# Performance work log

Hardware: AMD Instinct MI355X
Metric: run time of the kernel (lower is better)

## Reference

```python
import jax, jax.numpy as jnp
import numpy as np

SCALE = 0.125  # 1/sqrt(d_head=64)

def setup_inputs() -> dict:
    key = jax.random.key(0)
    kq, kk, kv = jax.random.split(key, 3)
    shape = (2, 12, 2048, 64)  # [batch, heads, seq, d_head]
    q = jax.random.normal(kq, shape, dtype=jnp.float32)
    k = jax.random.normal(kk, shape, dtype=jnp.float32)
    v = jax.random.normal(kv, shape, dtype=jnp.float32)
    return {"q": q, "k": k, "v": v}

def reference(q, k, v) -> jnp.ndarray:
    # atten = softmax(q @ k^T * scale); res = atten @ v
    scores = jnp.einsum('bhik,bhjk->bhij', q, k) * SCALE  # [B,H,S,S]
    atten = jax.nn.softmax(scores, axis=-1)
    # dropout is Identity (atten_dropout=None)
    res = jnp.einsum('bhij,bhjd->bhid', atten, v)  # [B,H,S,D]
    return res
```

## Files before the change

kernel.cpp:

```cpp
#include <hip/hip_runtime.h>
#include <math.h>

#define SEQ   2048
#define DH    64
#define NBH   24
#define QSCALE 0.18033688011112042f

typedef __attribute__((ext_vector_type(8))) short short8;
typedef __attribute__((ext_vector_type(4))) short short4v;
typedef __attribute__((ext_vector_type(4))) float f32x4;

#define MFMA32(a, b, c) __builtin_amdgcn_mfma_f32_16x16x32_bf16((a), (b), (c), 0, 0, 0)
#define MFMA16(a, b, c) __builtin_amdgcn_mfma_f32_16x16x16bf16_1k((a), (b), (c), 0, 0, 0)

__device__ __forceinline__ int cvtpk(float lo, float hi) {
    int r;
    asm("v_cvt_pk_bf16_f32 %0, %1, %2" : "=v"(r) : "v"(lo), "v"(hi));
    return r;
}

__global__ __launch_bounds__(256)
void cvt_all(const float* __restrict__ q, const float* __restrict__ k,
             const float* __restrict__ v,
             short* __restrict__ qb, short* __restrict__ kb,
             short* __restrict__ vt)
{
    __shared__ float tile[32][68];
    const int t  = threadIdx.x;
    const int bh = blockIdx.x;
    const int s0 = blockIdx.y * 32;
    const size_t base = ((size_t)bh * SEQ + s0) * DH;
    const size_t kbh  = (size_t)bh * SEQ * DH;

    #pragma unroll
    for (int i = 0; i < 2; ++i) {
        const int idx = i * 256 + t;
        float4 a = ((const float4*)(q + base))[idx];
        ((int2*)(qb + base))[idx] = make_int2(
            cvtpk(a.x * QSCALE, a.y * QSCALE),
            cvtpk(a.z * QSCALE, a.w * QSCALE));

        float4 b = ((const float4*)(k + base))[idx];
        {
            const int sl   = idx >> 4;
            const int fgrp = idx & 15;
            const int sblk = (s0 >> 4) + (sl >> 4);
            const int half = fgrp >> 3;
            const int quad = (fgrp >> 1) & 3;
            const int r04  = (fgrp & 1) * 4;
            short* p = kb + kbh + (size_t)sblk * 1024 + half * 512
                     + (quad * 16 + (sl & 15)) * 8 + r04;
            *(int2*)p = make_int2(cvtpk(b.x, b.y), cvtpk(b.z, b.w));
        }

        float4 c = ((const float4*)(v + base))[idx];
        const int sl = idx >> 4, cg = (idx & 15) * 4;
        *(float4*)(&tile[sl][cg]) = c;
    }
    __syncthreads();
    {
        const int dl = t >> 2;
        const int qq = t & 3;
        float f[8];
        #pragma unroll
        for (int r = 0; r < 4; ++r) {
            f[r]     = tile[qq * 4 + r][dl];
            f[4 + r] = tile[16 + qq * 4 + r][dl];
        }
        short8 pc;
        ((int*)&pc)[0] = cvtpk(f[0], f[1]);
        ((int*)&pc)[1] = cvtpk(f[2], f[3]);
        ((int*)&pc)[2] = cvtpk(f[4], f[5]);
        ((int*)&pc)[3] = cvtpk(f[6], f[7]);
        short* p = vt + kbh + (size_t)((s0 >> 5) * 4 + (dl >> 4)) * 512
                 + (qq * 16 + (dl & 15)) * 8;
        *(short8*)p = pc;
    }
}

__global__ __launch_bounds__(256, 3)
void attn_fwd(const short* __restrict__ qb, const short* __restrict__ kb,
              const short* __restrict__ vt, float* __restrict__ og)
{
    __shared__ float lds_o[4][2][64][17];
    __shared__ float lds_l[4][2][16];

    const int lane = threadIdx.x & 63;
    const int wave = threadIdx.x >> 6;
    const int quad = lane >> 4;
    const int l16  = lane & 15;
    const int lane8 = lane * 8;

    const int swz = (blockIdx.x & 7) * 192 + (blockIdx.x >> 3);
    const int bh  = swz >> 6;
    const int q0  = (swz & 63) * 32;

    const short* kbase = kb + (size_t)bh * SEQ * DH;
    const short* vbase = vt + (size_t)bh * DH * SEQ;

    short8 bq[2][2];
    #pragma unroll
    for (int qs = 0; qs < 2; ++qs) {
        const short* qrow = qb + ((size_t)(bh * SEQ + q0 + qs * 16 + l16)) * DH + quad * 8;
        bq[qs][0] = *(const short8*)(qrow);
        bq[qs][1] = *(const short8*)(qrow + 32);
    }

    f32x4 o[2][4];
    float l_i[2];
    #pragma unroll
    for (int qs = 0; qs < 2; ++qs) {
        l_i[qs] = 0.f;
        #pragma unroll
        for (int dt = 0; dt < 4; ++dt) o[qs][dt] = (f32x4){0.f, 0.f, 0.f, 0.f};
    }

    int k0 = wave * (SEQ / 4);
    short8 ka[8];
    #pragma unroll
    for (int mt = 0; mt < 4; ++mt) {
        const short* kc = kbase + (size_t)((k0 >> 4) + mt) * 1024 + lane8;
        ka[2 * mt]     = *(const short8*)(kc);
        ka[2 * mt + 1] = *(const short8*)(kc + 512);
    }

    #pragma unroll 1
    for (int iter = 0; iter < 8; ++iter, k0 += 64) {
        short8 av[2][4];
        #pragma unroll
        for (int pair = 0; pair < 2; ++pair)
            #pragma unroll
            for (int dt = 0; dt < 4; ++dt)
                av[pair][dt] = *(const short8*)(vbase
                    + (size_t)((((k0 >> 5) + pair) * 4) + dt) * 512 + lane8);

        short4v pb[2][4];

        #pragma unroll
        for (int qs = 0; qs < 2; ++qs) {
            f32x4 c[4];
            __builtin_amdgcn_s_setprio(1);
            #pragma unroll
            for (int mt = 0; mt < 4; ++mt) {
                f32x4 z = (f32x4){0.f, 0.f, 0.f, 0.f};
                z = MFMA32(ka[2 * mt],     bq[qs][0], z);
                z = MFMA32(ka[2 * mt + 1], bq[qs][1], z);
                c[mt] = z;
            }
            __builtin_amdgcn_s_setprio(0);

            if (qs == 1 && iter < 7) {
                const int k0n = k0 + 64;
                #pragma unroll
                for (int mt = 0; mt < 4; ++mt) {
                    const short* kc = kbase + (size_t)((k0n >> 4) + mt) * 1024 + lane8;
                    ka[2 * mt]     = *(const short8*)(kc);
                    ka[2 * mt + 1] = *(const short8*)(kc + 512);
                }
            }

            float rsm[4];
            #pragma unroll
            for (int mt = 0; mt < 4; ++mt) {
                float p[4];
                #pragma unroll
                for (int r = 0; r < 4; ++r)
                    p[r] = __builtin_amdgcn_exp2f(c[mt][r]);
                rsm[mt] = (p[0] + p[1]) + (p[2] + p[3]);
                int2 w = make_int2(cvtpk(p[0], p[1]), cvtpk(p[2], p[3]));
                pb[qs][mt] = __builtin_bit_cast(short4v, w);
            }
            l_i[qs] += (rsm[0] + rsm[1]) + (rsm[2] + rsm[3]);
        }

        __builtin_amdgcn_s_setprio(1);
        #pragma unroll
        for (int pair = 0; pair < 2; ++pair) {
            #pragma unroll
            for (int dt = 0; dt < 4; ++dt) {
                const short4v alo = __builtin_shufflevector(av[pair][dt], av[pair][dt], 0, 1, 2, 3);
                const short4v ahi = __builtin_shufflevector(av[pair][dt], av[pair][dt], 4, 5, 6, 7);
                #pragma unroll
                for (int qs = 0; qs < 2; ++qs) {
                    o[qs][dt] = MFMA16(alo, pb[qs][2 * pair],     o[qs][dt]);
                    o[qs][dt] = MFMA16(ahi, pb[qs][2 * pair + 1], o[qs][dt]);
                }
            }
        }
        __builtin_amdgcn_s_setprio(0);
    }

    #pragma unroll
    for (int qs = 0; qs < 2; ++qs) {
        float l = l_i[qs];
        l += __shfl_xor(l, 16, 64);
        l += __shfl_xor(l, 32, 64);
        l_i[qs] = l;
    }

    #pragma unroll
    for (int qs = 0; qs < 2; ++qs) {
        #pragma unroll
        for (int dt = 0; dt < 4; ++dt)
            #pragma unroll
            for (int r = 0; r < 4; ++r)
                lds_o[wave][qs][lane][dt * 4 + r] = o[qs][dt][r];
        if (quad == 0) lds_l[wave][qs][l16] = l_i[qs];
    }
    __syncthreads();
    #pragma unroll
    for (int j = 0; j < 2; ++j) {
        const int s  = wave * 2 + j;
        const int qs = s >> 2, dt = s & 3;
        const float L = (lds_l[0][qs][l16] + lds_l[1][qs][l16])
                      + (lds_l[2][qs][l16] + lds_l[3][qs][l16]);
        const float linv = 1.0f / L;
        f32x4 st;
        #pragma unroll
        for (int r = 0; r < 4; ++r)
            st[r] = ((lds_o[0][qs][lane][dt * 4 + r] + lds_o[1][qs][lane][dt * 4 + r])
                   + (lds_o[2][qs][lane][dt * 4 + r] + lds_o[3][qs][lane][dt * 4 + r]))
                  * linv;
        *(f32x4*)(og + ((size_t)(bh * SEQ + q0 + qs * 16 + l16)) * DH
                  + dt * 16 + quad * 4) = st;
    }
}

extern "C" void kernel_launch(void* const* d_in, const int* in_sizes, int n_in,
                              void* d_out, int out_size, void* d_ws, size_t ws_size,
                              hipStream_t stream)
{
    const float* q = (const float*)d_in[0];
    const float* k = (const float*)d_in[1];
    const float* v = (const float*)d_in[2];
    float* o = (float*)d_out;

    const size_t nelem = (size_t)NBH * SEQ * DH;
    short* qb  = (short*)d_ws;
    short* kbp = qb + nelem;
    short* vtp = kbp + nelem;

    cvt_all<<<dim3(NBH, SEQ / 32), 256, 0, stream>>>(q, k, v, qb, kbp, vtp);
    attn_fwd<<<dim3(NBH * (SEQ / 32)), 256, 0, stream>>>(qb, kbp, vtp, o);
}
```

Before: 118.0 us.

## Give each wave its own query tile over all keys instead of split-K

Previously the four waves of a block split the key range for a shared 32-query tile and merged their partial outputs through LDS. Now each wave owns a separate 32-query tile and walks all 2048 keys, so a block covers 128 queries and the LDS reduction and its block-wide sync are gone. A barrier at the top of each key iteration keeps the waves in step so they share K/V in cache. The cost is a four-times smaller grid (384 blocks), which lowers occupancy and latency hiding and leaves an uneven tail across CUs.

```diff
diff --git a/kernel.cpp b/kernel.cpp
--- a/kernel.cpp
+++ b/kernel.cpp
@@ -82,18 +82,15 @@
 void attn_fwd(const short* __restrict__ qb, const short* __restrict__ kb,
               const short* __restrict__ vt, float* __restrict__ og)
 {
-    __shared__ float lds_o[4][2][64][17];
-    __shared__ float lds_l[4][2][16];
-
     const int lane = threadIdx.x & 63;
     const int wave = threadIdx.x >> 6;
     const int quad = lane >> 4;
     const int l16  = lane & 15;
     const int lane8 = lane * 8;
 
-    const int swz = (blockIdx.x & 7) * 192 + (blockIdx.x >> 3);
-    const int bh  = swz >> 6;
-    const int q0  = (swz & 63) * 32;
+    const int swz = (blockIdx.x & 7) * 48 + (blockIdx.x >> 3);
+    const int bh  = swz >> 4;
+    const int q0  = (swz & 15) * 128 + wave * 32;
 
     const short* kbase = kb + (size_t)bh * SEQ * DH;
     const short* vbase = vt + (size_t)bh * DH * SEQ;
@@ -115,17 +112,19 @@
         for (int dt = 0; dt < 4; ++dt) o[qs][dt] = (f32x4){0.f, 0.f, 0.f, 0.f};
     }
 
-    int k0 = wave * (SEQ / 4);
+    int k0 = 0;
     short8 ka[8];
     #pragma unroll
     for (int mt = 0; mt < 4; ++mt) {
-        const short* kc = kbase + (size_t)((k0 >> 4) + mt) * 1024 + lane8;
+        const short* kc = kbase + (size_t)mt * 1024 + lane8;
         ka[2 * mt]     = *(const short8*)(kc);
         ka[2 * mt + 1] = *(const short8*)(kc + 512);
     }
 
     #pragma unroll 1
-    for (int iter = 0; iter < 8; ++iter, k0 += 64) {
+    for (int iter = 0; iter < 32; ++iter, k0 += 64) {
+        __builtin_amdgcn_s_barrier();
+
         short8 av[2][4];
         #pragma unroll
         for (int pair = 0; pair < 2; ++pair)
@@ -149,7 +148,7 @@
             }
             __builtin_amdgcn_s_setprio(0);
 
-            if (qs == 1 && iter < 7) {
+            if (qs == 1 && iter < 31) {
                 const int k0n = k0 + 64;
                 #pragma unroll
                 for (int mt = 0; mt < 4; ++mt) {
@@ -195,34 +194,15 @@
         float l = l_i[qs];
         l += __shfl_xor(l, 16, 64);
         l += __shfl_xor(l, 32, 64);
-        l_i[qs] = l;
-    }
-
-    #pragma unroll
-    for (int qs = 0; qs < 2; ++qs) {
-        #pragma unroll
-        for (int dt = 0; dt < 4; ++dt)
-            #pragma unroll
-            for (int r = 0; r < 4; ++r)
-                lds_o[wave][qs][lane][dt * 4 + r] = o[qs][dt][r];
-        if (quad == 0) lds_l[wave][qs][l16] = l_i[qs];
-    }
-    __syncthreads();
-    #pragma unroll
-    for (int j = 0; j < 2; ++j) {
-        const int s  = wave * 2 + j;
-        const int qs = s >> 2, dt = s & 3;
-        const float L = (lds_l[0][qs][l16] + lds_l[1][qs][l16])
-                      + (lds_l[2][qs][l16] + lds_l[3][qs][l16]);
-        const float linv = 1.0f / L;
-        f32x4 st;
-        #pragma unroll
-        for (int r = 0; r < 4; ++r)
-            st[r] = ((lds_o[0][qs][lane][dt * 4 + r] + lds_o[1][qs][lane][dt * 4 + r])
-                   + (lds_o[2][qs][lane][dt * 4 + r] + lds_o[3][qs][lane][dt * 4 + r]))
-                  * linv;
-        *(f32x4*)(og + ((size_t)(bh * SEQ + q0 + qs * 16 + l16)) * DH
-                  + dt * 16 + quad * 4) = st;
+        const float linv = 1.0f / l;
+        float* orow = og + ((size_t)(bh * SEQ + q0 + qs * 16 + l16)) * DH;
+        #pragma unroll
+        for (int dt = 0; dt < 4; ++dt) {
+            f32x4 st;
+            #pragma unroll
+            for (int r = 0; r < 4; ++r) st[r] = o[qs][dt][r] * linv;
+            *(f32x4*)(orow + dt * 16 + quad * 4) = st;
+        }
     }
 }
 
@@ -241,5 +221,5 @@
     short* vtp = kbp + nelem;
 
     cvt_all<<<dim3(NBH, SEQ / 32), 256, 0, stream>>>(q, k, v, qb, kbp, vtp);
-    attn_fwd<<<dim3(NBH * (SEQ / 32)), 256, 0, stream>>>(qb, kbp, vtp, o);
-}
+    attn_fwd<<<dim3(NBH * (SEQ / 128) * (128 / 128) * 16 / 16), 256, 0, stream>>>(qb, kbp, vtp, o);
+}
```

Result: slower. 136.2 us (+15.5%).
